# Kernel tuning notes

Measured on AMD Instinct MI355X. Metric: run time of the kernel, lower is better.

Reference implementation:

```python
import jax, jax.numpy as jnp
import numpy as np
from jax import lax

RHO = 1.0
LAMDA = 0.1
ADMM_ITERS = 10


def setup_inputs() -> dict:
    key = jax.random.key(0)
    k1, k2, k3, k4 = jax.random.split(key, 4)
    B, M, A, MULT = 2048, 512, 2048, 3
    S = A * MULT
    y = jax.random.normal(k1, (B, M), dtype=jnp.float32)
    x = jax.random.normal(k2, (B, A), dtype=jnp.float32)
    # measurement matrix buffer: randn(m, ambient)/sqrt(m)
    a = jax.random.normal(k3, (M, A), dtype=jnp.float32) / np.sqrt(M)
    # phi: kaiming_normal_ on (ambient*mult, ambient): std = sqrt(2/fan_in)
    phi = jax.random.normal(k4, (S, A), dtype=jnp.float32) * np.sqrt(2.0 / A)
    return {"y": y, "x": x, "a": a, "phi": phi}


def _shrink(v, thresh):
    return jnp.sign(v) * jnp.maximum(jnp.zeros_like(v), jnp.abs(v) - thresh)


def reference(y, x, a, phi):
    B = y.shape[0]
    x = x.reshape(B, -1)
    y = y.reshape(B, -1)
    min_x = jnp.min(x)
    max_x = jnp.max(x)
    S = phi.shape[0]
    u = jnp.zeros((B, S), dtype=y.dtype)
    z = jnp.zeros((B, S), dtype=y.dtype)

    # multiplier(rho): m = a^T a + rho * phi^T phi, LU-factor, invert L and U.
    m = a.T @ a + RHO * (phi.T @ phi)
    _, L, U = jax.scipy.linalg.lu(m)
    # NOTE: original uses einsum('aa,ba->ba', Linv, v) which contracts the
    # repeated index -> uses only diag(Linv) elementwise. Replicate exactly.
    dL = jnp.diagonal(jnp.linalg.inv(L))  # (A,) -- unit-lower -> ones
    dU = jnp.diagonal(jnp.linalg.inv(U))  # (A,)

    # x0 = einsum('am,bm->ba', a.T, y) = y @ a  -> (B, A)
    x0 = y @ a
    rho_phi = RHO * phi  # (S, A)

    def step(carry, _):
        u, z, _xh = carry
        # einsum('as,bs->ba', rho*phi.T, z-u) = (z-u) @ (rho*phi)
        x_L = dL * (x0 + (z - u) @ rho_phi)            # (B, A)
        x_hat = dU * x_L                                # (B, A)
        fxu = x_hat @ phi.T + u                         # (B, S)
        z_new = _shrink(fxu, LAMDA / RHO)
        u_new = u + fxu - z_new
        return (u_new, z_new, x_hat), None

    xh0 = jnp.zeros((B, x.shape[1]), dtype=y.dtype)
    (u, z, x_hat), _ = lax.scan(step, (u, z, xh0), None, length=ADMM_ITERS)
    return jnp.clip(x_hat, min_x, max_x)
```

## Files before the change

### kernel.cpp

```cpp
#include <hip/hip_runtime.h>

#define B_N 2048
#define M_N 512
#define A_N 2048
#define S_N 6144
#define SHRINK_T 0.1f
#define ADMM_ITERS 10

#define SPLIT_SCALE 512.0f
#define INV_SPLIT (1.0f / 512.0f)

typedef _Float16 v8h __attribute__((ext_vector_type(8)));
typedef _Float16 v4h __attribute__((ext_vector_type(4)));
typedef float v4f __attribute__((ext_vector_type(4)));

#define AS1 __attribute__((address_space(1)))
#define AS3 __attribute__((address_space(3)))

#define WAITCNT_VM8 0xF78
#define WAITCNT_VM0 0xF70

__device__ __forceinline__ float shrinkf(float v) {
  return copysignf(fmaxf(fabsf(v) - SHRINK_T, 0.f), v);
}

__device__ __forceinline__ unsigned fkey(float v) {
  unsigned b = __float_as_uint(v);
  return (b & 0x80000000u) ? ~b : (b | 0x80000000u);
}
__device__ __forceinline__ float key2f(unsigned k) {
  unsigned b = (k & 0x80000000u) ? (k & 0x7FFFFFFFu) : ~k;
  return __uint_as_float(b);
}

__device__ __forceinline__ void dma16(const _Float16* g, int ld, int r0, int k0,
                                      int slot, _Float16* region) {
  int m = slot >> 2;
  int k8 = (slot & 3) ^ ((m >> 1) & 3);
  const _Float16* gp = g + (size_t)(r0 + m) * ld + k0 + (k8 << 3);
  __builtin_amdgcn_global_load_lds((const AS1 void*)gp,
                                   (AS3 void*)(region + (size_t)(slot & ~63) * 8), 16, 0, 0);
}

template <int EPI, bool FZ>
__global__ __launch_bounds__(256, 2) void mgemm(
    const _Float16* __restrict__ Ah0, const _Float16* __restrict__ Al0, int ldA0, int K0,
    const _Float16* __restrict__ Bh0, const _Float16* __restrict__ Bl0, int ldB0,
    const _Float16* __restrict__ Ah1, const _Float16* __restrict__ Al1, int ldA1, int K1,
    const _Float16* __restrict__ Bh1, const _Float16* __restrict__ Bl1, int ldB1,
    float* __restrict__ C, int ldC, const float* __restrict__ dU,
    _Float16* __restrict__ Oh, _Float16* __restrict__ Ol, float* __restrict__ U,
    const unsigned* __restrict__ kk) {
  __shared__ _Float16 lds[2 * 16384];
  const int tid = threadIdx.x;
  const int i0 = blockIdx.y * 128, j0 = blockIdx.x * 128;
  const int lane = tid & 63, w = tid >> 6, wm = w >> 1, wn = w & 1;
  const int fb = (lane & 15) * 32 + (((lane >> 4) ^ ((lane >> 1) & 3)) << 3);

  v4f acc1[4][4], acc2[4][4];
  const v4f z4 = {0.f, 0.f, 0.f, 0.f};
#pragma unroll
  for (int tm = 0; tm < 4; ++tm)
#pragma unroll
    for (int tn = 0; tn < 4; ++tn) { acc1[tm][tn] = z4; acc2[tm][tn] = z4; }

  const int steps0 = K0 >> 5, steps1 = K1 >> 5, total = steps0 + steps1;

  auto issue = [&](int s, _Float16* buf) {
    const _Float16 *Ah, *Al, *Bh, *Bl;
    int ldA, ldB, k0;
    if (s < steps0) {
      Ah = Ah0; Al = Al0; Bh = Bh0; Bl = Bl0; ldA = ldA0; ldB = ldB0; k0 = s << 5;
    } else {
      Ah = Ah1; Al = Al1; Bh = Bh1; Bl = Bl1; ldA = ldA1; ldB = ldB1; k0 = (s - steps0) << 5;
    }
    dma16(Ah, ldA, i0, k0, tid,       buf);
    dma16(Ah, ldA, i0, k0, 256 + tid, buf);
    dma16(Al, ldA, i0, k0, tid,       buf + 4096);
    dma16(Al, ldA, i0, k0, 256 + tid, buf + 4096);
    dma16(Bh, ldB, j0, k0, tid,       buf + 8192);
    dma16(Bh, ldB, j0, k0, 256 + tid, buf + 8192);
    dma16(Bl, ldB, j0, k0, tid,       buf + 12288);
    dma16(Bl, ldB, j0, k0, 256 + tid, buf + 12288);
  };

  issue(0, lds);
  if (total > 1) issue(1, lds + 16384);

  for (int s = 0; s < total; ++s) {
    if (s + 1 < total) __builtin_amdgcn_s_waitcnt(WAITCNT_VM8);
    else               __builtin_amdgcn_s_waitcnt(WAITCNT_VM0);
    __asm__ volatile("" ::: "memory");
    __builtin_amdgcn_s_barrier();
    __asm__ volatile("" ::: "memory");

    const _Float16* L = lds + (s & 1) * 16384;
    v8h ah[4], al[4], bh[4], bl[4];
#pragma unroll
    for (int tm = 0; tm < 4; ++tm) {
      int off = (wm * 64 + tm * 16) * 32 + fb;
      ah[tm] = *(const v8h*)(L + off);
      al[tm] = *(const v8h*)(L + 4096 + off);
    }
#pragma unroll
    for (int tn = 0; tn < 4; ++tn) {
      int off = (wn * 64 + tn * 16) * 32 + fb;
      bh[tn] = *(const v8h*)(L + 8192 + off);
      bl[tn] = *(const v8h*)(L + 12288 + off);
    }
#pragma unroll
    for (int tm = 0; tm < 4; ++tm)
#pragma unroll
      for (int tn = 0; tn < 4; ++tn) {
        acc1[tm][tn] = __builtin_amdgcn_mfma_f32_16x16x32_f16(ah[tm], bh[tn], acc1[tm][tn], 0, 0, 0);
        v4f c2 = acc2[tm][tn];
        c2 = __builtin_amdgcn_mfma_f32_16x16x32_f16(ah[tm], bl[tn], c2, 0, 0, 0);
        c2 = __builtin_amdgcn_mfma_f32_16x16x32_f16(al[tm], bh[tn], c2, 0, 0, 0);
        acc2[tm][tn] = c2;
      }

    if (s + 2 < total) {
      __asm__ volatile("" ::: "memory");
      __builtin_amdgcn_s_barrier();
      __asm__ volatile("" ::: "memory");
      issue(s + 2, lds + (s & 1) * 16384);
    }
  }

  const int q = lane >> 4, lr = lane & 15;
  float mn = 0.f, mx = 0.f;
  if constexpr (EPI == 3) { mn = key2f(kk[0]); mx = key2f(kk[1]); }
#pragma unroll
  for (int tm = 0; tm < 4; ++tm)
#pragma unroll
    for (int tn = 0; tn < 4; ++tn) {
      int row0 = i0 + wm * 64 + tm * 16 + q * 4;
      int col = j0 + wn * 64 + tn * 16 + lr;
      if constexpr (EPI == 0) {
#pragma unroll
        for (int r = 0; r < 4; ++r) {
          size_t o = (size_t)(row0 + r) * ldC + col;
          C[o] = acc1[tm][tn][r] + acc2[tm][tn][r] * INV_SPLIT;
        }
      } else if constexpr (EPI == 1) {
        float du = dU[col];
#pragma unroll
        for (int r = 0; r < 4; ++r) {
          size_t o = (size_t)(row0 + r) * ldC + col;
          float v = (acc1[tm][tn][r] + acc2[tm][tn][r] * INV_SPLIT) * du;
          _Float16 h = (_Float16)v;
          Oh[o] = h;
          Ol[o] = (_Float16)((v - (float)h) * SPLIT_SCALE);
        }
      } else if constexpr (EPI == 3) {
        float du = dU[col];
#pragma unroll
        for (int r = 0; r < 4; ++r) {
          size_t o = (size_t)(row0 + r) * ldC + col;
          float v = (acc1[tm][tn][r] + acc2[tm][tn][r] * INV_SPLIT) * du;
          C[o] = fminf(fmaxf(v, mn), mx);
        }
      } else {
#pragma unroll
        for (int r = 0; r < 4; ++r) {
          size_t o = (size_t)(row0 + r) * ldC + col;
          float uo = FZ ? 0.f : U[o];
          float fx = acc1[tm][tn][r] + acc2[tm][tn][r] * INV_SPLIT + uo;
          float zn = shrinkf(fx);
          float un = uo + fx - zn;
          U[o] = un;
          float zu = zn - un;
          _Float16 h = (_Float16)zu;
          Oh[o] = h;
          Ol[o] = (_Float16)((zu - (float)h) * SPLIT_SCALE);
        }
      }
    }
}

__global__ __launch_bounds__(256) void split_kernel(const float* __restrict__ s,
                                                    _Float16* __restrict__ h,
                                                    _Float16* __restrict__ l, int n4) {
  for (int i = blockIdx.x * 256 + threadIdx.x; i < n4; i += gridDim.x * 256) {
    float4 v = ((const float4*)s)[i];
    v4h hh, ll;
    hh.x = (_Float16)v.x; ll.x = (_Float16)((v.x - (float)hh.x) * SPLIT_SCALE);
    hh.y = (_Float16)v.y; ll.y = (_Float16)((v.y - (float)hh.y) * SPLIT_SCALE);
    hh.z = (_Float16)v.z; ll.z = (_Float16)((v.z - (float)hh.z) * SPLIT_SCALE);
    hh.w = (_Float16)v.w; ll.w = (_Float16)((v.w - (float)hh.w) * SPLIT_SCALE);
    ((v4h*)h)[i] = hh;
    ((v4h*)l)[i] = ll;
  }
}

__global__ __launch_bounds__(256) void tsplit_kernel(const float* __restrict__ src, int R, int C,
                                                     _Float16* __restrict__ h,
                                                     _Float16* __restrict__ l) {
  __shared__ float t[32][33];
  int br = blockIdx.y * 32, bc = blockIdx.x * 32;
  int r = threadIdx.x >> 3, c4 = (threadIdx.x & 7) * 4;
  float4 v = *(const float4*)(src + (size_t)(br + r) * C + bc + c4);
  t[r][c4 + 0] = v.x; t[r][c4 + 1] = v.y; t[r][c4 + 2] = v.z; t[r][c4 + 3] = v.w;
  __syncthreads();
  int a = threadIdx.x >> 3, r4 = (threadIdx.x & 7) * 4;
  float x0 = t[r4 + 0][a], x1 = t[r4 + 1][a], x2 = t[r4 + 2][a], x3 = t[r4 + 3][a];
  v4h hh, ll;
  hh.x = (_Float16)x0; ll.x = (_Float16)((x0 - (float)hh.x) * SPLIT_SCALE);
  hh.y = (_Float16)x1; ll.y = (_Float16)((x1 - (float)hh.y) * SPLIT_SCALE);
  hh.z = (_Float16)x2; ll.z = (_Float16)((x2 - (float)hh.z) * SPLIT_SCALE);
  hh.w = (_Float16)x3; ll.w = (_Float16)((x3 - (float)hh.w) * SPLIT_SCALE);
  size_t o = (size_t)(bc + a) * R + br + r4;
  *(v4h*)(h + o) = hh;
  *(v4h*)(l + o) = ll;
}

__global__ __launch_bounds__(256) void chol64_kernel(float* __restrict__ mm,
                                                     float* __restrict__ dU, int kb) {
  __shared__ float Ad[64][65];
  int tid = threadIdx.x;
  for (int e = tid; e < 64 * 64; e += 256) {
    int r = e >> 6, c = e & 63;
    Ad[r][c] = mm[(size_t)(kb + r) * A_N + kb + c];
  }
  __syncthreads();
  for (int j = 0; j < 64; ++j) {
    if (tid == 0) Ad[j][j] = sqrtf(Ad[j][j]);
    __syncthreads();
    if (tid > j && tid < 64) Ad[tid][j] /= Ad[j][j];
    __syncthreads();
    int i = j + 1 + (tid >> 2);
    int q = tid & 3;
    if (i < 64) {
      float lij = Ad[i][j];
      for (int t = j + 1 + q; t <= i; t += 4)
        Ad[i][t] = fmaf(-lij, Ad[t][j], Ad[i][t]);
    }
    __syncthreads();
  }
  if (tid < 64) {
    float d = Ad[tid][tid];
    dU[kb + tid] = 1.0f / (d * d);
  }
  for (int e = tid; e < 64 * 64; e += 256) {
    int r = e >> 6, c = e & 63;
    if (c <= r) mm[(size_t)(kb + r) * A_N + kb + c] = Ad[r][c];
  }
}

__global__ __launch_bounds__(256) void trsm64_kernel(float* __restrict__ mm, int kb) {
  __shared__ float Ls[64][65];
  int tid = threadIdx.x;
  for (int e = tid; e < 64 * 64; e += 256) {
    int r = e >> 6, c = e & 63;
    Ls[r][c] = mm[(size_t)(kb + r) * A_N + kb + c];
  }
  __syncthreads();
  int row = kb + 64 + blockIdx.x * 256 + tid;
  if (row >= A_N) return;
  float v[64];
  float* gr = mm + (size_t)row * A_N + kb;
#pragma unroll
  for (int qq = 0; qq < 16; ++qq) {
    float4 t = *(const float4*)(gr + qq * 4);
    v[qq * 4 + 0] = t.x; v[qq * 4 + 1] = t.y;
    v[qq * 4 + 2] = t.z; v[qq * 4 + 3] = t.w;
  }
#pragma unroll
  for (int j = 0; j < 64; ++j) {
    float s = v[j];
#pragma unroll
    for (int t = 0; t < j; ++t) s = fmaf(-v[t], Ls[j][t], s);
    v[j] = s / Ls[j][j];
  }
#pragma unroll
  for (int qq = 0; qq < 16; ++qq)
    *(float4*)(gr + qq * 4) =
        make_float4(v[qq * 4 + 0], v[qq * 4 + 1], v[qq * 4 + 2], v[qq * 4 + 3]);
}

__global__ __launch_bounds__(256) void syrk64_kernel(float* __restrict__ mm, int kb) {
  __shared__ float As[16 * 64];
  __shared__ float Bs[16 * 64];
  int tid = threadIdx.x, tx = tid & 15, ty = tid >> 4;
  int base = kb + 64;
  int i0 = base + blockIdx.y * 64;
  int j0 = base + blockIdx.x * 64;
  float acc[4][4] = {{0.f}};
  for (int k0 = 0; k0 < 64; k0 += 16) {
    __syncthreads();
    {
      int ii = tid >> 2, k4 = (tid & 3) * 4;
      float4 vv = *(const float4*)(mm + (size_t)(i0 + ii) * A_N + kb + k0 + k4);
      As[(k4 + 0) * 64 + ii] = vv.x; As[(k4 + 1) * 64 + ii] = vv.y;
      As[(k4 + 2) * 64 + ii] = vv.z; As[(k4 + 3) * 64 + ii] = vv.w;
      float4 ww = *(const float4*)(mm + (size_t)(j0 + ii) * A_N + kb + k0 + k4);
      Bs[(k4 + 0) * 64 + ii] = ww.x; Bs[(k4 + 1) * 64 + ii] = ww.y;
      Bs[(k4 + 2) * 64 + ii] = ww.z; Bs[(k4 + 3) * 64 + ii] = ww.w;
    }
    __syncthreads();
#pragma unroll
    for (int k = 0; k < 16; ++k) {
      float4 a0 = *(const float4*)(As + k * 64 + ty * 4);
      float4 b0 = *(const float4*)(Bs + k * 64 + tx * 4);
      float av[4] = {a0.x, a0.y, a0.z, a0.w};
      float bv[4] = {b0.x, b0.y, b0.z, b0.w};
#pragma unroll
      for (int i = 0; i < 4; ++i)
#pragma unroll
        for (int j = 0; j < 4; ++j) acc[i][j] = fmaf(av[i], bv[j], acc[i][j]);
    }
  }
#pragma unroll
  for (int i = 0; i < 4; ++i) {
    float* p = mm + (size_t)(i0 + ty * 4 + i) * A_N + j0 + tx * 4;
    float4 c = *(const float4*)p;
    c.x -= acc[i][0]; c.y -= acc[i][1]; c.z -= acc[i][2]; c.w -= acc[i][3];
    *(float4*)p = c;
  }
}

__global__ void minmax_init(unsigned* keys) {
  keys[0] = 0xFFFFFFFFu;
  keys[1] = 0u;
}

__global__ __launch_bounds__(256) void minmax_kernel(const float* __restrict__ x,
                                                     unsigned* __restrict__ keys, int n4) {
  unsigned mn = 0xFFFFFFFFu, mx = 0u;
  for (int i = blockIdx.x * 256 + threadIdx.x; i < n4; i += gridDim.x * 256) {
    float4 v = ((const float4*)x)[i];
    unsigned k0 = fkey(v.x), k1 = fkey(v.y), k2 = fkey(v.z), k3 = fkey(v.w);
    mn = min(mn, min(min(k0, k1), min(k2, k3)));
    mx = max(mx, max(max(k0, k1), max(k2, k3)));
  }
  for (int o = 32; o > 0; o >>= 1) {
    mn = min(mn, (unsigned)__shfl_down((int)mn, o));
    mx = max(mx, (unsigned)__shfl_down((int)mx, o));
  }
  if ((threadIdx.x & 63) == 0) {
    atomicMin(&keys[0], mn);
    atomicMax(&keys[1], mx);
  }
}

extern "C" void kernel_launch(void* const* d_in, const int* in_sizes, int n_in,
                              void* d_out, int out_size, void* d_ws, size_t ws_size,
                              hipStream_t stream) {
  const float* y   = (const float*)d_in[0];
  const float* x   = (const float*)d_in[1];
  const float* a   = (const float*)d_in[2];
  const float* phi = (const float*)d_in[3];
  float* out = (float*)d_out;

  char* ws = (char*)d_ws;
  size_t off = 0;
  auto alloc = [&](size_t bytes) -> void* {
    void* p = ws + off;
    off = (off + bytes + 255) & ~(size_t)255;
    return p;
  };
  float* mm = (float*)alloc(sizeof(float) * (size_t)A_N * A_N);
  float* u  = (float*)alloc(sizeof(float) * (size_t)B_N * S_N);
  float* dU = (float*)alloc(sizeof(float) * A_N);
  unsigned* keys = (unsigned*)alloc(sizeof(unsigned) * 2);
  _Float16* phi_h  = (_Float16*)alloc(2 * (size_t)S_N * A_N);
  _Float16* phi_l  = (_Float16*)alloc(2 * (size_t)S_N * A_N);
  _Float16* phiT_h = (_Float16*)alloc(2 * (size_t)A_N * S_N);
  _Float16* phiT_l = (_Float16*)alloc(2 * (size_t)A_N * S_N);
  _Float16* aT_h   = (_Float16*)alloc(2 * (size_t)A_N * M_N);
  _Float16* aT_l   = (_Float16*)alloc(2 * (size_t)A_N * M_N);
  _Float16* y_h    = (_Float16*)alloc(2 * (size_t)B_N * M_N);
  _Float16* y_l    = (_Float16*)alloc(2 * (size_t)B_N * M_N);
  _Float16* zu_h   = (_Float16*)alloc(2 * (size_t)B_N * S_N);
  _Float16* zu_l   = (_Float16*)alloc(2 * (size_t)B_N * S_N);
  _Float16* xh_h   = (_Float16*)alloc(2 * (size_t)B_N * A_N);
  _Float16* xh_l   = (_Float16*)alloc(2 * (size_t)B_N * A_N);

  minmax_init<<<1, 1, 0, stream>>>(keys);
  minmax_kernel<<<1024, 256, 0, stream>>>(x, keys, (B_N * A_N) / 4);

  split_kernel<<<2048, 256, 0, stream>>>(phi, phi_h, phi_l, (S_N * A_N) / 4);
  split_kernel<<<512, 256, 0, stream>>>(y, y_h, y_l, (B_N * M_N) / 4);
  tsplit_kernel<<<dim3(A_N / 32, S_N / 32), 256, 0, stream>>>(phi, S_N, A_N, phiT_h, phiT_l);
  tsplit_kernel<<<dim3(A_N / 32, M_N / 32), 256, 0, stream>>>(a, M_N, A_N, aT_h, aT_l);

  mgemm<0, false><<<dim3(A_N / 128, A_N / 128), 256, 0, stream>>>(
      aT_h, aT_l, M_N, M_N, aT_h, aT_l, M_N,
      phiT_h, phiT_l, S_N, S_N, phiT_h, phiT_l, S_N,
      mm, A_N, nullptr, nullptr, nullptr, nullptr, nullptr);

  for (int kb = 0; kb < A_N; kb += 64) {
    chol64_kernel<<<1, 256, 0, stream>>>(mm, dU, kb);
    int rows = A_N - kb - 64;
    if (rows > 0) {
      trsm64_kernel<<<(rows + 255) / 256, 256, 0, stream>>>(mm, kb);
      syrk64_kernel<<<dim3(rows / 64, rows / 64), 256, 0, stream>>>(mm, kb);
    }
  }

  for (int it = 0; it < ADMM_ITERS; ++it) {
    int Kzu = (it == 0) ? 0 : S_N;
    if (it < ADMM_ITERS - 1) {
      mgemm<1, false><<<dim3(A_N / 128, B_N / 128), 256, 0, stream>>>(
          zu_h, zu_l, S_N, Kzu, phiT_h, phiT_l, S_N,
          y_h, y_l, M_N, M_N, aT_h, aT_l, M_N,
          nullptr, A_N, dU, xh_h, xh_l, nullptr, nullptr);
    } else {
      mgemm<3, false><<<dim3(A_N / 128, B_N / 128), 256, 0, stream>>>(
          zu_h, zu_l, S_N, Kzu, phiT_h, phiT_l, S_N,
          y_h, y_l, M_N, M_N, aT_h, aT_l, M_N,
          out, A_N, dU, nullptr, nullptr, nullptr, keys);
    }
    if (it < ADMM_ITERS - 1) {
      if (it == 0)
        mgemm<2, true><<<dim3(S_N / 128, B_N / 128), 256, 0, stream>>>(
            xh_h, xh_l, A_N, A_N, phi_h, phi_l, A_N,
            nullptr, nullptr, 0, 0, nullptr, nullptr, 0,
            nullptr, S_N, nullptr, zu_h, zu_l, u, nullptr);
      else
        mgemm<2, false><<<dim3(S_N / 128, B_N / 128), 256, 0, stream>>>(
            xh_h, xh_l, A_N, A_N, phi_h, phi_l, A_N,
            nullptr, nullptr, 0, 0, nullptr, nullptr, 0,
            nullptr, S_N, nullptr, zu_h, zu_l, u, nullptr);
    }
  }
}
```

Baseline: 6.503 ms.

## Fuse phi split/transpose, skip dead U store, halve SYRK blocks, tighten Cholesky pivot

Merges the two phi preprocessing kernels into one that reads phi once and writes both the split and transposed split copies. Skips writing U in the last z/u update, whose U is never read again. Early-exits the upper-triangle blocks in the trailing SYRK update, since only the lower triangle is consumed. Folds the pivot sqrt and column scaling in chol64 into one phase using rsqrt, which drops a barrier per column but adds a small rounding difference.

```diff
diff --git a/kernel.cpp b/kernel.cpp
--- a/kernel.cpp
+++ b/kernel.cpp
@@ -42,7 +42,7 @@
                                    (AS3 void*)(region + (size_t)(slot & ~63) * 8), 16, 0, 0);
 }
 
-template <int EPI, bool FZ>
+template <int EPI, bool FZ, bool WU>
 __global__ __launch_bounds__(256, 2) void mgemm(
     const _Float16* __restrict__ Ah0, const _Float16* __restrict__ Al0, int ldA0, int K0,
     const _Float16* __restrict__ Bh0, const _Float16* __restrict__ Bl0, int ldB0,
@@ -168,7 +168,7 @@
           float fx = acc1[tm][tn][r] + acc2[tm][tn][r] * INV_SPLIT + uo;
           float zn = shrinkf(fx);
           float un = uo + fx - zn;
-          U[o] = un;
+          if constexpr (WU) U[o] = un;
           float zu = zn - un;
           _Float16 h = (_Float16)zu;
           Oh[o] = h;
@@ -191,6 +191,39 @@
     ((v4h*)h)[i] = hh;
     ((v4h*)l)[i] = ll;
   }
+}
+
+__global__ __launch_bounds__(256) void phiprep_kernel(const float* __restrict__ src,
+                                                      _Float16* __restrict__ h,
+                                                      _Float16* __restrict__ l,
+                                                      _Float16* __restrict__ th,
+                                                      _Float16* __restrict__ tl) {
+  __shared__ float t[32][33];
+  int br = blockIdx.y * 32, bc = blockIdx.x * 32;
+  int r = threadIdx.x >> 3, c4 = (threadIdx.x & 7) * 4;
+  float4 v = *(const float4*)(src + (size_t)(br + r) * A_N + bc + c4);
+  t[r][c4 + 0] = v.x; t[r][c4 + 1] = v.y; t[r][c4 + 2] = v.z; t[r][c4 + 3] = v.w;
+  {
+    v4h hh, ll;
+    hh.x = (_Float16)v.x; ll.x = (_Float16)((v.x - (float)hh.x) * SPLIT_SCALE);
+    hh.y = (_Float16)v.y; ll.y = (_Float16)((v.y - (float)hh.y) * SPLIT_SCALE);
+    hh.z = (_Float16)v.z; ll.z = (_Float16)((v.z - (float)hh.z) * SPLIT_SCALE);
+    hh.w = (_Float16)v.w; ll.w = (_Float16)((v.w - (float)hh.w) * SPLIT_SCALE);
+    size_t o = (size_t)(br + r) * A_N + bc + c4;
+    *(v4h*)(h + o) = hh;
+    *(v4h*)(l + o) = ll;
+  }
+  __syncthreads();
+  int a = threadIdx.x >> 3, r4 = (threadIdx.x & 7) * 4;
+  float x0 = t[r4 + 0][a], x1 = t[r4 + 1][a], x2 = t[r4 + 2][a], x3 = t[r4 + 3][a];
+  v4h hh, ll;
+  hh.x = (_Float16)x0; ll.x = (_Float16)((x0 - (float)hh.x) * SPLIT_SCALE);
+  hh.y = (_Float16)x1; ll.y = (_Float16)((x1 - (float)hh.y) * SPLIT_SCALE);
+  hh.z = (_Float16)x2; ll.z = (_Float16)((x2 - (float)hh.z) * SPLIT_SCALE);
+  hh.w = (_Float16)x3; ll.w = (_Float16)((x3 - (float)hh.w) * SPLIT_SCALE);
+  size_t o = (size_t)(bc + a) * S_N + br + r4;
+  *(v4h*)(th + o) = hh;
+  *(v4h*)(tl + o) = ll;
 }
 
 __global__ __launch_bounds__(256) void tsplit_kernel(const float* __restrict__ src, int R, int C,
@@ -224,9 +257,11 @@
   }
   __syncthreads();
   for (int j = 0; j < 64; ++j) {
-    if (tid == 0) Ad[j][j] = sqrtf(Ad[j][j]);
-    __syncthreads();
-    if (tid > j && tid < 64) Ad[tid][j] /= Ad[j][j];
+    if (tid < 64) {
+      float piv = Ad[j][j];
+      if (tid == j) Ad[j][j] = sqrtf(piv);
+      else if (tid > j) Ad[tid][j] *= rsqrtf(piv);
+    }
     __syncthreads();
     int i = j + 1 + (tid >> 2);
     int q = tid & 3;
@@ -279,6 +314,7 @@
 }
 
 __global__ __launch_bounds__(256) void syrk64_kernel(float* __restrict__ mm, int kb) {
+  if (blockIdx.x > blockIdx.y) return;
   __shared__ float As[16 * 64];
   __shared__ float Bs[16 * 64];
   int tid = threadIdx.x, tx = tid & 15, ty = tid >> 4;
@@ -379,12 +415,12 @@
   minmax_init<<<1, 1, 0, stream>>>(keys);
   minmax_kernel<<<1024, 256, 0, stream>>>(x, keys, (B_N * A_N) / 4);
 
-  split_kernel<<<2048, 256, 0, stream>>>(phi, phi_h, phi_l, (S_N * A_N) / 4);
+  phiprep_kernel<<<dim3(A_N / 32, S_N / 32), 256, 0, stream>>>(phi, phi_h, phi_l,
+                                                               phiT_h, phiT_l);
   split_kernel<<<512, 256, 0, stream>>>(y, y_h, y_l, (B_N * M_N) / 4);
-  tsplit_kernel<<<dim3(A_N / 32, S_N / 32), 256, 0, stream>>>(phi, S_N, A_N, phiT_h, phiT_l);
   tsplit_kernel<<<dim3(A_N / 32, M_N / 32), 256, 0, stream>>>(a, M_N, A_N, aT_h, aT_l);
 
-  mgemm<0, false><<<dim3(A_N / 128, A_N / 128), 256, 0, stream>>>(
+  mgemm<0, false, false><<<dim3(A_N / 128, A_N / 128), 256, 0, stream>>>(
       aT_h, aT_l, M_N, M_N, aT_h, aT_l, M_N,
       phiT_h, phiT_l, S_N, S_N, phiT_h, phiT_l, S_N,
       mm, A_N, nullptr, nullptr, nullptr, nullptr, nullptr);
@@ -401,24 +437,29 @@
   for (int it = 0; it < ADMM_ITERS; ++it) {
     int Kzu = (it == 0) ? 0 : S_N;
     if (it < ADMM_ITERS - 1) {
-      mgemm<1, false><<<dim3(A_N / 128, B_N / 128), 256, 0, stream>>>(
+      mgemm<1, false, false><<<dim3(A_N / 128, B_N / 128), 256, 0, stream>>>(
           zu_h, zu_l, S_N, Kzu, phiT_h, phiT_l, S_N,
           y_h, y_l, M_N, M_N, aT_h, aT_l, M_N,
           nullptr, A_N, dU, xh_h, xh_l, nullptr, nullptr);
     } else {
-      mgemm<3, false><<<dim3(A_N / 128, B_N / 128), 256, 0, stream>>>(
+      mgemm<3, false, false><<<dim3(A_N / 128, B_N / 128), 256, 0, stream>>>(
           zu_h, zu_l, S_N, Kzu, phiT_h, phiT_l, S_N,
           y_h, y_l, M_N, M_N, aT_h, aT_l, M_N,
           out, A_N, dU, nullptr, nullptr, nullptr, keys);
     }
     if (it < ADMM_ITERS - 1) {
       if (it == 0)
-        mgemm<2, true><<<dim3(S_N / 128, B_N / 128), 256, 0, stream>>>(
+        mgemm<2, true, true><<<dim3(S_N / 128, B_N / 128), 256, 0, stream>>>(
+            xh_h, xh_l, A_N, A_N, phi_h, phi_l, A_N,
+            nullptr, nullptr, 0, 0, nullptr, nullptr, 0,
+            nullptr, S_N, nullptr, zu_h, zu_l, u, nullptr);
+      else if (it < ADMM_ITERS - 2)
+        mgemm<2, false, true><<<dim3(S_N / 128, B_N / 128), 256, 0, stream>>>(
             xh_h, xh_l, A_N, A_N, phi_h, phi_l, A_N,
             nullptr, nullptr, 0, 0, nullptr, nullptr, 0,
             nullptr, S_N, nullptr, zu_h, zu_l, u, nullptr);
       else
-        mgemm<2, false><<<dim3(S_N / 128, B_N / 128), 256, 0, stream>>>(
+        mgemm<2, false, false><<<dim3(S_N / 128, B_N / 128), 256, 0, stream>>>(
             xh_h, xh_l, A_N, A_N, phi_h, phi_l, A_N,
             nullptr, nullptr, 0, 0, nullptr, nullptr, 0,
             nullptr, S_N, nullptr, zu_h, zu_l, u, nullptr);
```

Result: slower. 6.656 ms (+2.3%).
